# Kernel tuning notes

Hardware: AMD Instinct MI355X
Metric: run time of the kernel (lower is better)

## Reference

```python
import jax, jax.numpy as jnp
import numpy as np

N = 100000      # nodes
E = 640000      # edges
VOCAB = 100     # Embedding(num_embeddings=100)
EMB = 10        # embed_dim
H = 128         # GCN hidden width


def gcn_conv(x, W, b, src, dst, n):
    """PyG GCNConv: linear (no bias) -> add self loops -> sym-normalized scatter-add -> +bias."""
    x = x @ W                                  # [n, out]
    loop = jnp.arange(n, dtype=src.dtype)
    src2 = jnp.concatenate([src, loop])        # [E+n]
    dst2 = jnp.concatenate([dst, loop])
    deg = jax.ops.segment_sum(jnp.ones_like(dst2, dtype=x.dtype), dst2, num_segments=n)
    dinv = jnp.where(deg > 0, jax.lax.rsqrt(deg), 0.0)
    norm = dinv[src2] * dinv[dst2]             # [E+n]
    out = jax.ops.segment_sum(x[src2] * norm[:, None], dst2, num_segments=n)
    return out + b


def setup_inputs() -> dict:
    key = jax.random.key(0)
    ks = jax.random.split(key, 9)
    x = jax.random.randint(ks[0], (N, 1), 0, VOCAB, dtype=jnp.int32)
    edge_index = jax.random.randint(ks[1], (2, E), 0, N, dtype=jnp.int32)
    batch = jnp.zeros((N,), dtype=jnp.int32)
    emb = jax.random.normal(ks[2], (VOCAB, EMB), dtype=jnp.float32)
    W1 = jax.random.normal(ks[3], (EMB, H), dtype=jnp.float32) * 0.1
    b1 = jnp.zeros((H,), dtype=jnp.float32)
    W2 = jax.random.normal(ks[4], (H, H), dtype=jnp.float32) * 0.1
    b2 = jnp.zeros((H,), dtype=jnp.float32)
    W3 = jax.random.normal(ks[5], (H, 1), dtype=jnp.float32) * 0.1
    b3 = jnp.zeros((1,), dtype=jnp.float32)
    return {"x": x, "edge_index": edge_index, "batch": batch,
            "emb": emb, "W1": W1, "b1": b1, "W2": W2, "b2": b2, "W3": W3, "b3": b3}


def reference(x, edge_index, batch, emb, W1, b1, W2, b2, W3, b3):
    # eval mode: dropout(p=0.5) is identity
    h = emb[x[:, 0]]                           # [N, EMB] embedding lookup + squeeze
    src, dst = edge_index[0], edge_index[1]
    n = h.shape[0]
    h = jax.nn.relu(gcn_conv(h, W1, b1, src, dst, n))   # [N, 128]
    h = jax.nn.relu(gcn_conv(h, W2, b2, src, dst, n))   # [N, 128]
    out = jax.nn.sigmoid((h @ W3 + b3).reshape(-1))      # [N]
    return out
```

## Files before the change

kernel.cpp:

```cpp
#include <hip/hip_runtime.h>
#include <math.h>

#define HDIM 128
#define EMBD 10
#define CAP  64
#define ZSTRIDE 136

typedef __attribute__((ext_vector_type(8))) short short8;
typedef __attribute__((ext_vector_type(8))) unsigned short ushort8;
typedef __attribute__((ext_vector_type(4))) float float4a;

__device__ inline ushort bf16_rne(float f) {
    unsigned u = __float_as_uint(f);
    unsigned r = (u + 0x7fffu + ((u >> 16) & 1u)) >> 16;
    return (ushort)r;
}
__device__ inline float bf16_to_f(ushort u) {
    return __uint_as_float(((unsigned)u) << 16);
}

__global__ void k_prep(const float* __restrict__ emb, const float* __restrict__ W1,
                       const float* __restrict__ W2, float* __restrict__ T,
                       ushort* __restrict__ W2t, int* __restrict__ cnt,
                       int N, int vocab) {
    int t = blockIdx.x * 256 + threadIdx.x;
    if (t < N) cnt[t] = 0;
    if (t < vocab * HDIM) {
        int c = t >> 7, f = t & 127;
        float s = 0.f;
#pragma unroll
        for (int k = 0; k < EMBD; ++k) s += emb[c * EMBD + k] * W1[k * HDIM + f];
        T[t] = s;
    }
    if (t < HDIM * HDIM) {
        int n = t >> 7, k = t & 127;
        W2t[t] = bf16_rne(W2[k * HDIM + n]);
    }
}

__global__ void k_fill(const int* __restrict__ src, const int* __restrict__ dst,
                       int* __restrict__ cnt, int* __restrict__ slot, int E) {
    int e = blockIdx.x * blockDim.x + threadIdx.x;
    if (e >= E) return;
    int d = dst[e];
    int p = atomicAdd(&cnt[d], 1);
    if (p < CAP) slot[(size_t)d * CAP + p] = src[e];
}

__global__ void k_gather1(const int* __restrict__ slot, const int* __restrict__ cnt,
                          const int* __restrict__ x, const float* __restrict__ T,
                          const float* __restrict__ b1, ushort* __restrict__ A, int N) {
    int tid = blockIdx.x * 256 + threadIdx.x;
    int v = tid >> 4, q = tid & 15;
    if (v >= N) return;
    int deg = cnt[v];
    int m = min(deg, CAP);
    float acc[8] = {0.f, 0.f, 0.f, 0.f, 0.f, 0.f, 0.f, 0.f};
    for (int base = 0; base < m; base += 16) {
        int j = base + q;
        int cls = 0; float w = 0.f;
        if (j < m) {
            int s = slot[(size_t)v * CAP + j];
            cls = x[s];
            w = rsqrtf((float)cnt[s] + 1.0f);
        }
        int lim = min(m - base, 16);
#pragma unroll 2
        for (int t = 0; t < lim; ++t) {
            int c    = __shfl(cls, t, 16);
            float ww = __shfl(w, t, 16);
            const float* tr = T + c * HDIM + q * 8;
            float4 t0 = *(const float4*)tr;
            float4 t1 = *(const float4*)(tr + 4);
            acc[0] += ww * t0.x; acc[1] += ww * t0.y;
            acc[2] += ww * t0.z; acc[3] += ww * t0.w;
            acc[4] += ww * t1.x; acc[5] += ww * t1.y;
            acc[6] += ww * t1.z; acc[7] += ww * t1.w;
        }
    }
    float dv = rsqrtf((float)deg + 1.0f);
    float dd = dv * dv;
    const float* tr = T + x[v] * HDIM + q * 8;
    float4 t0 = *(const float4*)tr;
    float4 t1 = *(const float4*)(tr + 4);
    float4 bb0 = *(const float4*)(b1 + q * 8);
    float4 bb1 = *(const float4*)(b1 + q * 8 + 4);
    float ts[8] = {t0.x, t0.y, t0.z, t0.w, t1.x, t1.y, t1.z, t1.w};
    float bb[8] = {bb0.x, bb0.y, bb0.z, bb0.w, bb1.x, bb1.y, bb1.z, bb1.w};
    ushort8 o;
#pragma unroll
    for (int k = 0; k < 8; ++k)
        o[k] = bf16_rne(fmaxf(dv * acc[k] + dd * ts[k] + bb[k], 0.f));
    *(ushort8*)(A + (size_t)v * HDIM + q * 8) = o;
}

__global__ __launch_bounds__(256) void k_conv2(const int* __restrict__ slot,
                                               const int* __restrict__ cnt,
                                               const ushort* __restrict__ A,
                                               const ushort* __restrict__ W2t,
                                               const float* __restrict__ b2,
                                               const float* __restrict__ W3,
                                               const float* __restrict__ b3,
                                               float* __restrict__ out, int N) {
    __shared__ ushort Z[4][16 * ZSTRIDE];
    int lane = threadIdx.x & 63;
    int wid  = threadIdx.x >> 6;
    int q16  = lane & 15;
    int g4   = lane >> 4;
    int tile = blockIdx.x * 4 + wid;
    int v0   = tile * 16;

    if (v0 < N) {
        for (int r = 0; r < 4; ++r) {
            int vr = v0 + r * 4 + g4;
            int v = min(vr, N - 1);
            int deg = cnt[v];
            int m = min(deg, CAP);
            float acc[8] = {0.f, 0.f, 0.f, 0.f, 0.f, 0.f, 0.f, 0.f};
            for (int base = 0; base < m; base += 16) {
                int j = base + q16;
                int sj = 0; float wj = 0.f;
                if (j < m) {
                    sj = slot[(size_t)v * CAP + j];
                    wj = rsqrtf((float)cnt[sj] + 1.0f);
                }
                int lim = min(m - base, 16);
                int t = 0;
                for (; t + 4 <= lim; t += 4) {
                    int s0 = __shfl(sj, t, 16),     s1 = __shfl(sj, t + 1, 16);
                    int s2 = __shfl(sj, t + 2, 16), s3 = __shfl(sj, t + 3, 16);
                    float w0 = __shfl(wj, t, 16),     w1 = __shfl(wj, t + 1, 16);
                    float w2 = __shfl(wj, t + 2, 16), w3v = __shfl(wj, t + 3, 16);
                    ushort8 y0 = *(const ushort8*)(A + (size_t)s0 * HDIM + q16 * 8);
                    ushort8 y1 = *(const ushort8*)(A + (size_t)s1 * HDIM + q16 * 8);
                    ushort8 y2 = *(const ushort8*)(A + (size_t)s2 * HDIM + q16 * 8);
                    ushort8 y3 = *(const ushort8*)(A + (size_t)s3 * HDIM + q16 * 8);
#pragma unroll
                    for (int k = 0; k < 8; ++k) acc[k] += w0 * bf16_to_f(y0[k]);
#pragma unroll
                    for (int k = 0; k < 8; ++k) acc[k] += w1 * bf16_to_f(y1[k]);
#pragma unroll
                    for (int k = 0; k < 8; ++k) acc[k] += w2 * bf16_to_f(y2[k]);
#pragma unroll
                    for (int k = 0; k < 8; ++k) acc[k] += w3v * bf16_to_f(y3[k]);
                }
                for (; t < lim; ++t) {
                    int s0 = __shfl(sj, t, 16);
                    float w0 = __shfl(wj, t, 16);
                    ushort8 y0 = *(const ushort8*)(A + (size_t)s0 * HDIM + q16 * 8);
#pragma unroll
                    for (int k = 0; k < 8; ++k) acc[k] += w0 * bf16_to_f(y0[k]);
                }
            }
            float dv = rsqrtf((float)deg + 1.0f);
            float dd = dv * dv;
            ushort8 ys = *(const ushort8*)(A + (size_t)v * HDIM + q16 * 8);
            ushort8 z;
#pragma unroll
            for (int k = 0; k < 8; ++k)
                z[k] = bf16_rne(dv * acc[k] + dd * bf16_to_f(ys[k]));
            *(ushort8*)&Z[wid][(r * 4 + g4) * ZSTRIDE + q16 * 8] = z;
        }
    }
    __syncthreads();
    if (v0 >= N) return;

    short8 af[4];
#pragma unroll
    for (int kt = 0; kt < 4; ++kt)
        af[kt] = *(const short8*)&Z[wid][q16 * ZSTRIDE + kt * 32 + g4 * 8];

    float4a accD[8];
#pragma unroll
    for (int nt = 0; nt < 8; ++nt) accD[nt] = (float4a){0.f, 0.f, 0.f, 0.f};
#pragma unroll
    for (int nt = 0; nt < 8; ++nt) {
        const ushort* bp = W2t + (size_t)(nt * 16 + q16) * HDIM + g4 * 8;
#pragma unroll
        for (int kt = 0; kt < 4; ++kt) {
            short8 bf = *(const short8*)(bp + kt * 32);
            accD[nt] = __builtin_amdgcn_mfma_f32_16x16x32_bf16(af[kt], bf, accD[nt], 0, 0, 0);
        }
    }

    float p[4] = {0.f, 0.f, 0.f, 0.f};
#pragma unroll
    for (int nt = 0; nt < 8; ++nt) {
        int col = nt * 16 + q16;
        float bc = b2[col], wc = W3[col];
#pragma unroll
        for (int r = 0; r < 4; ++r)
            p[r] += fmaxf(accD[nt][r] + bc, 0.f) * wc;
    }
#pragma unroll
    for (int off = 1; off < 16; off <<= 1) {
#pragma unroll
        for (int r = 0; r < 4; ++r) p[r] += __shfl_xor(p[r], off, 16);
    }
    if (q16 == 0) {
        float b3v = b3[0];
#pragma unroll
        for (int r = 0; r < 4; ++r) {
            int row = v0 + g4 * 4 + r;
            if (row < N) out[row] = 1.f / (1.f + expf(-(p[r] + b3v)));
        }
    }
}

extern "C" void kernel_launch(void* const* d_in, const int* in_sizes, int n_in,
                              void* d_out, int out_size, void* d_ws, size_t ws_size,
                              hipStream_t stream) {
    const int*   x    = (const int*)d_in[0];
    const int*   ei   = (const int*)d_in[1];
    const float* emb  = (const float*)d_in[3];
    const float* W1   = (const float*)d_in[4];
    const float* b1   = (const float*)d_in[5];
    const float* W2   = (const float*)d_in[6];
    const float* b2   = (const float*)d_in[7];
    const float* W3   = (const float*)d_in[8];
    const float* b3   = (const float*)d_in[9];
    float*       out  = (float*)d_out;

    int N = in_sizes[0];
    int E = in_sizes[1] / 2;
    int vocab = in_sizes[3] / EMBD;
    const int* src = ei;
    const int* dst = ei + E;

    char* w = (char*)d_ws;
    float*  T    = (float*)w;   w += (size_t)vocab * HDIM * 4;
    ushort* A    = (ushort*)w;  w += (size_t)N * HDIM * 2;
    ushort* W2t  = (ushort*)w;  w += (size_t)HDIM * HDIM * 2;
    int*    cnt  = (int*)w;     w += (size_t)N * 4;
    int*    slot = (int*)w;     w += (size_t)N * CAP * 4;

    int prep_elems = N;
    if (vocab * HDIM > prep_elems) prep_elems = vocab * HDIM;
    if (HDIM * HDIM > prep_elems) prep_elems = HDIM * HDIM;
    k_prep<<<(prep_elems + 255) / 256, 256, 0, stream>>>(emb, W1, W2, T, W2t, cnt, N, vocab);
    k_fill<<<(E + 255) / 256, 256, 0, stream>>>(src, dst, cnt, slot, E);

    int gblocks = (int)(((long long)N * 16 + 255) / 256);
    k_gather1<<<gblocks, 256, 0, stream>>>(slot, cnt, x, T, b1, A, N);

    int ntiles = (N + 15) / 16;
    k_conv2<<<(ntiles + 3) / 4, 256, 0, stream>>>(slot, cnt, A, W2t, b2, W3, b3, out, N);
}
```

Before: 199.3 us.

## Batch neighbor gathers with fixed 16-wide unrolled loads and split conv2 across waves

Both gather kernels now issue the first 16 neighbor-row loads at once, unrolled and branch-free. The self-loop term is folded into an otherwise idle lane's slot, which raises memory-level parallelism for the typical degree (~6.4). The embedding-projection table is stored as bf16 to halve the gather traffic. conv2 is restructured so each 256-thread block handles 16 nodes with one node per 16-lane group, and the four waves split the 128 output columns of the MFMA, reducing partial sums through shared memory. This trades redundant padded loads and an extra block-level sync for more concurrent loads and smaller per-wave register use.

```diff
diff --git a/kernel.cpp b/kernel.cpp
--- a/kernel.cpp
+++ b/kernel.cpp
@@ -20,7 +20,7 @@
 }
 
 __global__ void k_prep(const float* __restrict__ emb, const float* __restrict__ W1,
-                       const float* __restrict__ W2, float* __restrict__ T,
+                       const float* __restrict__ W2, ushort* __restrict__ Tb,
                        ushort* __restrict__ W2t, int* __restrict__ cnt,
                        int N, int vocab) {
     int t = blockIdx.x * 256 + threadIdx.x;
@@ -30,7 +30,7 @@
         float s = 0.f;
 #pragma unroll
         for (int k = 0; k < EMBD; ++k) s += emb[c * EMBD + k] * W1[k * HDIM + f];
-        T[t] = s;
+        Tb[t] = bf16_rne(s);
     }
     if (t < HDIM * HDIM) {
         int n = t >> 7, k = t & 127;
@@ -47,50 +47,72 @@
     if (p < CAP) slot[(size_t)d * CAP + p] = src[e];
 }
 
-__global__ void k_gather1(const int* __restrict__ slot, const int* __restrict__ cnt,
-                          const int* __restrict__ x, const float* __restrict__ T,
-                          const float* __restrict__ b1, ushort* __restrict__ A, int N) {
+__global__ __launch_bounds__(256) void k_gather1(const int* __restrict__ slot,
+                                                 const int* __restrict__ cnt,
+                                                 const int* __restrict__ x,
+                                                 const ushort* __restrict__ Tb,
+                                                 const float* __restrict__ b1,
+                                                 ushort* __restrict__ A, int N) {
     int tid = blockIdx.x * 256 + threadIdx.x;
     int v = tid >> 4, q = tid & 15;
     if (v >= N) return;
     int deg = cnt[v];
     int m = min(deg, CAP);
+    float dv = rsqrtf((float)deg + 1.0f);
+
+    int cq = x[v]; float wq = 0.f;
+    if (q < m) {
+        int s = slot[(size_t)v * CAP + q];
+        cq = x[s];
+        wq = rsqrtf((float)cnt[s] + 1.0f);
+    } else if (q == m) {
+        wq = dv;
+    }
+    int   cs[16]; float ws[16];
+#pragma unroll
+    for (int t = 0; t < 16; ++t) {
+        cs[t] = __shfl(cq, t, 16);
+        ws[t] = __shfl(wq, t, 16);
+    }
+    ushort8 rows[16];
+#pragma unroll
+    for (int t = 0; t < 16; ++t)
+        rows[t] = *(const ushort8*)(Tb + (size_t)cs[t] * HDIM + q * 8);
     float acc[8] = {0.f, 0.f, 0.f, 0.f, 0.f, 0.f, 0.f, 0.f};
-    for (int base = 0; base < m; base += 16) {
+#pragma unroll
+    for (int t = 0; t < 16; ++t) {
+#pragma unroll
+        for (int k = 0; k < 8; ++k) acc[k] += ws[t] * bf16_to_f(rows[t][k]);
+    }
+    for (int base = 16; base < m; base += 16) {
         int j = base + q;
-        int cls = 0; float w = 0.f;
+        int cj = x[v]; float wj = 0.f;
         if (j < m) {
             int s = slot[(size_t)v * CAP + j];
-            cls = x[s];
-            w = rsqrtf((float)cnt[s] + 1.0f);
-        }
-        int lim = min(m - base, 16);
-#pragma unroll 2
-        for (int t = 0; t < lim; ++t) {
-            int c    = __shfl(cls, t, 16);
-            float ww = __shfl(w, t, 16);
-            const float* tr = T + c * HDIM + q * 8;
-            float4 t0 = *(const float4*)tr;
-            float4 t1 = *(const float4*)(tr + 4);
-            acc[0] += ww * t0.x; acc[1] += ww * t0.y;
-            acc[2] += ww * t0.z; acc[3] += ww * t0.w;
-            acc[4] += ww * t1.x; acc[5] += ww * t1.y;
-            acc[6] += ww * t1.z; acc[7] += ww * t1.w;
-        }
-    }
-    float dv = rsqrtf((float)deg + 1.0f);
-    float dd = dv * dv;
-    const float* tr = T + x[v] * HDIM + q * 8;
-    float4 t0 = *(const float4*)tr;
-    float4 t1 = *(const float4*)(tr + 4);
+            cj = x[s];
+            wj = rsqrtf((float)cnt[s] + 1.0f);
+        }
+#pragma unroll
+        for (int t = 0; t < 16; ++t) {
+            int c = __shfl(cj, t, 16);
+            float ww = __shfl(wj, t, 16);
+            ushort8 y = *(const ushort8*)(Tb + (size_t)c * HDIM + q * 8);
+#pragma unroll
+            for (int k = 0; k < 8; ++k) acc[k] += ww * bf16_to_f(y[k]);
+        }
+    }
+    if (m >= 16) {
+        ushort8 y = *(const ushort8*)(Tb + (size_t)x[v] * HDIM + q * 8);
+#pragma unroll
+        for (int k = 0; k < 8; ++k) acc[k] += dv * bf16_to_f(y[k]);
+    }
     float4 bb0 = *(const float4*)(b1 + q * 8);
     float4 bb1 = *(const float4*)(b1 + q * 8 + 4);
-    float ts[8] = {t0.x, t0.y, t0.z, t0.w, t1.x, t1.y, t1.z, t1.w};
     float bb[8] = {bb0.x, bb0.y, bb0.z, bb0.w, bb1.x, bb1.y, bb1.z, bb1.w};
     ushort8 o;
 #pragma unroll
     for (int k = 0; k < 8; ++k)
-        o[k] = bf16_rne(fmaxf(dv * acc[k] + dd * ts[k] + bb[k], 0.f));
+        o[k] = bf16_rne(fmaxf(dv * acc[k] + bb[k], 0.f));
     *(ushort8*)(A + (size_t)v * HDIM + q * 8) = o;
 }
 
@@ -102,108 +124,106 @@
                                                const float* __restrict__ W3,
                                                const float* __restrict__ b3,
                                                float* __restrict__ out, int N) {
-    __shared__ ushort Z[4][16 * ZSTRIDE];
-    int lane = threadIdx.x & 63;
-    int wid  = threadIdx.x >> 6;
-    int q16  = lane & 15;
-    int g4   = lane >> 4;
-    int tile = blockIdx.x * 4 + wid;
-    int v0   = tile * 16;
-
-    if (v0 < N) {
-        for (int r = 0; r < 4; ++r) {
-            int vr = v0 + r * 4 + g4;
-            int v = min(vr, N - 1);
-            int deg = cnt[v];
-            int m = min(deg, CAP);
-            float acc[8] = {0.f, 0.f, 0.f, 0.f, 0.f, 0.f, 0.f, 0.f};
-            for (int base = 0; base < m; base += 16) {
-                int j = base + q16;
-                int sj = 0; float wj = 0.f;
-                if (j < m) {
-                    sj = slot[(size_t)v * CAP + j];
-                    wj = rsqrtf((float)cnt[sj] + 1.0f);
-                }
-                int lim = min(m - base, 16);
-                int t = 0;
-                for (; t + 4 <= lim; t += 4) {
-                    int s0 = __shfl(sj, t, 16),     s1 = __shfl(sj, t + 1, 16);
-                    int s2 = __shfl(sj, t + 2, 16), s3 = __shfl(sj, t + 3, 16);
-                    float w0 = __shfl(wj, t, 16),     w1 = __shfl(wj, t + 1, 16);
-                    float w2 = __shfl(wj, t + 2, 16), w3v = __shfl(wj, t + 3, 16);
-                    ushort8 y0 = *(const ushort8*)(A + (size_t)s0 * HDIM + q16 * 8);
-                    ushort8 y1 = *(const ushort8*)(A + (size_t)s1 * HDIM + q16 * 8);
-                    ushort8 y2 = *(const ushort8*)(A + (size_t)s2 * HDIM + q16 * 8);
-                    ushort8 y3 = *(const ushort8*)(A + (size_t)s3 * HDIM + q16 * 8);
-#pragma unroll
-                    for (int k = 0; k < 8; ++k) acc[k] += w0 * bf16_to_f(y0[k]);
-#pragma unroll
-                    for (int k = 0; k < 8; ++k) acc[k] += w1 * bf16_to_f(y1[k]);
-#pragma unroll
-                    for (int k = 0; k < 8; ++k) acc[k] += w2 * bf16_to_f(y2[k]);
-#pragma unroll
-                    for (int k = 0; k < 8; ++k) acc[k] += w3v * bf16_to_f(y3[k]);
-                }
-                for (; t < lim; ++t) {
-                    int s0 = __shfl(sj, t, 16);
-                    float w0 = __shfl(wj, t, 16);
-                    ushort8 y0 = *(const ushort8*)(A + (size_t)s0 * HDIM + q16 * 8);
-#pragma unroll
-                    for (int k = 0; k < 8; ++k) acc[k] += w0 * bf16_to_f(y0[k]);
-                }
-            }
-            float dv = rsqrtf((float)deg + 1.0f);
-            float dd = dv * dv;
-            ushort8 ys = *(const ushort8*)(A + (size_t)v * HDIM + q16 * 8);
-            ushort8 z;
-#pragma unroll
-            for (int k = 0; k < 8; ++k)
-                z[k] = bf16_rne(dv * acc[k] + dd * bf16_to_f(ys[k]));
-            *(ushort8*)&Z[wid][(r * 4 + g4) * ZSTRIDE + q16 * 8] = z;
-        }
-    }
+    __shared__ ushort Z[16 * ZSTRIDE];
+    __shared__ float pbuf[4][16];
+    int tid = threadIdx.x;
+    int g = tid >> 4, q = tid & 15;
+    int v0 = blockIdx.x * 16;
+    int v = min(v0 + g, N - 1);
+
+    int deg = cnt[v];
+    int m = min(deg, CAP);
+    float dv = rsqrtf((float)deg + 1.0f);
+
+    int sq = v; float wq = 0.f;
+    if (q < m) {
+        sq = slot[(size_t)v * CAP + q];
+        wq = rsqrtf((float)cnt[sq] + 1.0f);
+    } else if (q == m) {
+        wq = dv;
+    }
+    int   ss[16]; float ws[16];
+#pragma unroll
+    for (int t = 0; t < 16; ++t) {
+        ss[t] = __shfl(sq, t, 16);
+        ws[t] = __shfl(wq, t, 16);
+    }
+    ushort8 rows[16];
+#pragma unroll
+    for (int t = 0; t < 16; ++t)
+        rows[t] = *(const ushort8*)(A + (size_t)ss[t] * HDIM + q * 8);
+    float acc[8] = {0.f, 0.f, 0.f, 0.f, 0.f, 0.f, 0.f, 0.f};
+#pragma unroll
+    for (int t = 0; t < 16; ++t) {
+#pragma unroll
+        for (int k = 0; k < 8; ++k) acc[k] += ws[t] * bf16_to_f(rows[t][k]);
+    }
+    for (int base = 16; base < m; base += 16) {
+        int j = base + q;
+        int sj = v; float wj = 0.f;
+        if (j < m) {
+            sj = slot[(size_t)v * CAP + j];
+            wj = rsqrtf((float)cnt[sj] + 1.0f);
+        }
+#pragma unroll
+        for (int t = 0; t < 16; ++t) {
+            int s = __shfl(sj, t, 16);
+            float ww = __shfl(wj, t, 16);
+            ushort8 y = *(const ushort8*)(A + (size_t)s * HDIM + q * 8);
+#pragma unroll
+            for (int k = 0; k < 8; ++k) acc[k] += ww * bf16_to_f(y[k]);
+        }
+    }
+    if (m >= 16) {
+        ushort8 y = *(const ushort8*)(A + (size_t)v * HDIM + q * 8);
+#pragma unroll
+        for (int k = 0; k < 8; ++k) acc[k] += dv * bf16_to_f(y[k]);
+    }
+    ushort8 z;
+#pragma unroll
+    for (int k = 0; k < 8; ++k) z[k] = bf16_rne(dv * acc[k]);
+    *(ushort8*)&Z[g * ZSTRIDE + q * 8] = z;
     __syncthreads();
-    if (v0 >= N) return;
-
+
+    int lane = tid & 63, w = tid >> 6;
+    int l15 = lane & 15, g4 = lane >> 4;
     short8 af[4];
 #pragma unroll
     for (int kt = 0; kt < 4; ++kt)
-        af[kt] = *(const short8*)&Z[wid][q16 * ZSTRIDE + kt * 32 + g4 * 8];
-
-    float4a accD[8];
-#pragma unroll
-    for (int nt = 0; nt < 8; ++nt) accD[nt] = (float4a){0.f, 0.f, 0.f, 0.f};
-#pragma unroll
-    for (int nt = 0; nt < 8; ++nt) {
-        const ushort* bp = W2t + (size_t)(nt * 16 + q16) * HDIM + g4 * 8;
+        af[kt] = *(const short8*)&Z[l15 * ZSTRIDE + kt * 32 + g4 * 8];
+
+    float pr[4] = {0.f, 0.f, 0.f, 0.f};
+#pragma unroll
+    for (int i = 0; i < 2; ++i) {
+        int nt = w * 2 + i;
+        int col = nt * 16 + l15;
+        const ushort* bp = W2t + (size_t)col * HDIM + g4 * 8;
+        float4a accD = {0.f, 0.f, 0.f, 0.f};
 #pragma unroll
         for (int kt = 0; kt < 4; ++kt) {
             short8 bf = *(const short8*)(bp + kt * 32);
-            accD[nt] = __builtin_amdgcn_mfma_f32_16x16x32_bf16(af[kt], bf, accD[nt], 0, 0, 0);
-        }
-    }
-
-    float p[4] = {0.f, 0.f, 0.f, 0.f};
-#pragma unroll
-    for (int nt = 0; nt < 8; ++nt) {
-        int col = nt * 16 + q16;
+            accD = __builtin_amdgcn_mfma_f32_16x16x32_bf16(af[kt], bf, accD, 0, 0, 0);
+        }
         float bc = b2[col], wc = W3[col];
 #pragma unroll
         for (int r = 0; r < 4; ++r)
-            p[r] += fmaxf(accD[nt][r] + bc, 0.f) * wc;
+            pr[r] += fmaxf(accD[r] + bc, 0.f) * wc;
     }
 #pragma unroll
     for (int off = 1; off < 16; off <<= 1) {
 #pragma unroll
-        for (int r = 0; r < 4; ++r) p[r] += __shfl_xor(p[r], off, 16);
-    }
-    if (q16 == 0) {
-        float b3v = b3[0];
-#pragma unroll
-        for (int r = 0; r < 4; ++r) {
-            int row = v0 + g4 * 4 + r;
-            if (row < N) out[row] = 1.f / (1.f + expf(-(p[r] + b3v)));
-        }
+        for (int r = 0; r < 4; ++r) pr[r] += __shfl_xor(pr[r], off, 16);
+    }
+    if (l15 == 0) {
+#pragma unroll
+        for (int r = 0; r < 4; ++r) pbuf[w][g4 * 4 + r] = pr[r];
+    }
+    __syncthreads();
+    if (tid < 16) {
+        int row = tid;
+        float s = pbuf[0][row] + pbuf[1][row] + pbuf[2][row] + pbuf[3][row];
+        int vr = v0 + row;
+        if (vr < N) out[vr] = 1.f / (1.f + expf(-(s + b3[0])));
     }
 }
 
@@ -228,7 +248,7 @@
     const int* dst = ei + E;
 
     char* w = (char*)d_ws;
-    float*  T    = (float*)w;   w += (size_t)vocab * HDIM * 4;
+    ushort* Tb   = (ushort*)w;  w += (size_t)vocab * HDIM * 2;
     ushort* A    = (ushort*)w;  w += (size_t)N * HDIM * 2;
     ushort* W2t  = (ushort*)w;  w += (size_t)HDIM * HDIM * 2;
     int*    cnt  = (int*)w;     w += (size_t)N * 4;
@@ -237,12 +257,12 @@
     int prep_elems = N;
     if (vocab * HDIM > prep_elems) prep_elems = vocab * HDIM;
     if (HDIM * HDIM > prep_elems) prep_elems = HDIM * HDIM;
-    k_prep<<<(prep_elems + 255) / 256, 256, 0, stream>>>(emb, W1, W2, T, W2t, cnt, N, vocab);
+    k_prep<<<(prep_elems + 255) / 256, 256, 0, stream>>>(emb, W1, W2, Tb, W2t, cnt, N, vocab);
     k_fill<<<(E + 255) / 256, 256, 0, stream>>>(src, dst, cnt, slot, E);
 
     int gblocks = (int)(((long long)N * 16 + 255) / 256);
-    k_gather1<<<gblocks, 256, 0, stream>>>(slot, cnt, x, T, b1, A, N);
-
-    int ntiles = (N + 15) / 16;
-    k_conv2<<<(ntiles + 3) / 4, 256, 0, stream>>>(slot, cnt, A, W2t, b2, W3, b3, out, N);
-}
+    k_gather1<<<gblocks, 256, 0, stream>>>(slot, cnt, x, Tb, b1, A, N);
+
+    int cblocks = (N + 15) / 16;
+    k_conv2<<<cblocks, 256, 0, stream>>>(slot, cnt, A, W2t, b2, W3, b3, out, N);
+}
```

Result: faster. 184.0 us (-7.7%).
